# Performance work log

Hardware: AMD Instinct MI355X
Metric: run time of the kernel (lower is better)

Reference implementation:

```python
import jax, jax.numpy as jnp
import numpy as np

N_NODES = 50000
EMB = 256
HEADS = 8
NEG_SLOPE = 0.2


def gat_conv(x, src, dst, W, a_src, a_dst, b, num_nodes):
    # x: [N, Din]; W: [Din, H, F]; a_src/a_dst: [H, F]; b: [H*F]
    h = jnp.einsum('nd,dhf->nhf', x, W)                      # [N, H, F]
    al_s = jnp.sum(h * a_src, axis=-1)                       # [N, H]
    al_d = jnp.sum(h * a_dst, axis=-1)                       # [N, H]
    logits = jax.nn.leaky_relu(al_s[src] + al_d[dst], NEG_SLOPE)  # [E, H]
    # segment softmax over incoming edges of each destination node
    m = jax.ops.segment_max(logits, dst, num_segments=num_nodes)  # [N, H]
    e = jnp.exp(logits - m[dst])                              # [E, H]
    z = jax.ops.segment_sum(e, dst, num_segments=num_nodes)   # [N, H]
    alpha = e / (z[dst] + 1e-16)                              # [E, H]
    msg = h[src] * alpha[..., None]                           # [E, H, F]
    out = jax.ops.segment_sum(msg, dst, num_segments=num_nodes)  # [N, H, F]
    return out.reshape(num_nodes, -1) + b


def setup_inputs() -> dict:
    key = jax.random.key(0)
    ks = jax.random.split(key, 10)
    F1 = EMB // HEADS  # 32
    x = jax.random.normal(ks[0], (N_NODES, EMB), dtype=jnp.float32)
    edge_index = jax.random.randint(ks[1], (2, 800000), 0, N_NODES, dtype=jnp.int64)
    s1 = 1.0 / np.sqrt(EMB)
    W1 = jax.random.normal(ks[2], (EMB, HEADS, F1), dtype=jnp.float32) * s1
    a_src1 = jax.random.normal(ks[3], (HEADS, F1), dtype=jnp.float32) * s1
    a_dst1 = jax.random.normal(ks[4], (HEADS, F1), dtype=jnp.float32) * s1
    b1 = jnp.zeros((HEADS * F1,), dtype=jnp.float32)
    W2 = jax.random.normal(ks[5], (EMB, 1, EMB), dtype=jnp.float32) * s1
    a_src2 = jax.random.normal(ks[6], (1, EMB), dtype=jnp.float32) * s1
    a_dst2 = jax.random.normal(ks[7], (1, EMB), dtype=jnp.float32) * s1
    b2 = jnp.zeros((EMB,), dtype=jnp.float32)
    return {"x": x, "edge_index": edge_index,
            "W1": W1, "a_src1": a_src1, "a_dst1": a_dst1, "b1": b1,
            "W2": W2, "a_src2": a_src2, "a_dst2": a_dst2, "b2": b2}


def reference(x, edge_index, W1, a_src1, a_dst1, b1, W2, a_src2, a_dst2, b2):
    n = x.shape[0]
    loops = jnp.arange(n, dtype=edge_index.dtype)
    src = jnp.concatenate([edge_index[0], loops])
    dst = jnp.concatenate([edge_index[1], loops])
    h = gat_conv(x, src, dst, W1, a_src1, a_dst1, b1, n)   # [N, EMB]
    out = gat_conv(h, src, dst, W2, a_src2, a_dst2, b2, n)  # [N, EMB]
    return out
```

## Files before the change

kernel.cpp:

```cpp
#include <hip/hip_runtime.h>
#include <hip/hip_bf16.h>

typedef unsigned short u16;
typedef unsigned int   u32;

typedef __attribute__((ext_vector_type(8))) short s16x8;
typedef __attribute__((ext_vector_type(8))) unsigned short u16x8;
typedef __attribute__((ext_vector_type(4))) float f32x4;

#define CAP 64

__device__ __forceinline__ float b2f(u16 u) {
    union { u32 i; float f; } v; v.i = ((u32)u) << 16; return v.f;
}
__device__ __forceinline__ u16 f2b(float f) {
    union { float f; u32 i; } v; v.f = f;
    u32 u = v.i;
    u32 r = (u + 0x7fffu + ((u >> 16) & 1u)) >> 16;
    return (u16)r;
}

__device__ __forceinline__ int detect_f32(const u16* xw) {
    int t = threadIdx.x & 63;
    u16 w = xw[2 * t];
    int e = (w >> 7) & 0xFF;
    bool sane = (e >= 112 && e <= 131);
    unsigned long long m1 = __ballot(sane);
    return (__popcll(m1) >= 32) ? 0 : 1;
}

__device__ __forceinline__ int edge_at(const int* __restrict__ ei, int i64f, long long j) {
    return i64f ? ei[2 * j] : ei[(size_t)j];
}

__device__ __forceinline__ u16x8 loadA8(const void* __restrict__ A, size_t eoff, int f32f) {
    if (f32f) {
        const float* p = (const float*)A + eoff;
        float4 v0 = *(const float4*)p;
        float4 v1 = *(const float4*)(p + 4);
        u16x8 r;
        r[0] = f2b(v0.x); r[1] = f2b(v0.y); r[2] = f2b(v0.z); r[3] = f2b(v0.w);
        r[4] = f2b(v1.x); r[5] = f2b(v1.y); r[6] = f2b(v1.z); r[7] = f2b(v1.w);
        return r;
    }
    return *(const u16x8*)((const u16*)A + eoff);
}

__global__ __launch_bounds__(256) void prep(const void* __restrict__ x,
                                            const int* __restrict__ ei,
                                            const void* __restrict__ W1, const void* __restrict__ W2,
                                            const void* p0, const void* p1, const void* p2,
                                            const void* p3, const void* p4, const void* p5,
                                            u16* __restrict__ wt1, u16* __restrict__ wt2,
                                            u16* __restrict__ sv,
                                            int* __restrict__ cur, u16* __restrict__ csr,
                                            int* __restrict__ flags, u16* __restrict__ hp,
                                            int ZB, int CF, int NN) {
    int b = blockIdx.x, t = threadIdx.x;
    int f32f = detect_f32((const u16*)x);
    if (b < 512) {
        const void* W = (b < 256) ? W1 : W2;
        u16* Wt = (b < 256) ? wt1 : wt2;
        int k = b & 255;
        u16 v = f32f ? f2b(((const float*)W)[k * 256 + t]) : ((const u16*)W)[k * 256 + t];
        Wt[t * 256 + k] = v;
        return;
    }
    b -= 512;
    if (b == 0) {
        const void* ps[6] = {p0, p1, p2, p3, p4, p5};
#pragma unroll
        for (int j = 0; j < 6; j++) {
            u16 v = f32f ? f2b(((const float*)ps[j])[t]) : ((const u16*)ps[j])[t];
            sv[j * 256 + t] = v;
        }
        hp[(size_t)NN * 256 + t] = 0;
        if (t < 64) {
            bool hz = (ei[2 * t + 1] == 0);
            unsigned long long m2 = __ballot(hz);
            if (t == 0) {
                flags[0] = f32f;
                flags[1] = (m2 == ~0ull) ? 1 : 0;
            }
        }
        return;
    }
    b -= 1;
    if (b < ZB) {
        int i = b * 256 + t;
        if (i < (NN + 3) / 4) ((int4*)cur)[i] = make_int4(0, 0, 0, 0);
        return;
    }
    b -= ZB;
    if (b < CF) {
        int i = b * 256 + t;
        int pat = (NN & 0xFFFF) | (NN << 16);
        if (i < NN * (CAP / 8)) ((int4*)csr)[i] = make_int4(pat, pat, pat, pat);
        return;
    }
}

__global__ __launch_bounds__(256) void fill_csr(const int* __restrict__ ei,
                                                int* __restrict__ cur,
                                                u16* __restrict__ csr, int E, int ET,
                                                const int* __restrict__ flags) {
    int i = blockIdx.x * 256 + threadIdx.x;
    if (i >= ET) return;
    int i64f = flags[1];
    int s, d;
    if (i < E) { s = edge_at(ei, i64f, i); d = edge_at(ei, i64f, (long long)E + i); }
    else       { s = d = i - E; }
    int p = atomicAdd(&cur[d], 1);
    if (p < CAP) csr[d * CAP + p] = (u16)s;
}

__global__ __launch_bounds__(256) void gemm_tiled(const void* __restrict__ A,
                                                  const u16* __restrict__ Bt,
                                                  u16* __restrict__ C, int M,
                                                  const int* __restrict__ flags, int dynA) {
    __shared__ u16 sA[128 * 32];
    __shared__ u16 sB[128 * 32];
    int f32a = dynA ? flags[0] : 0;
    int tid = threadIdx.x;
    int mt = blockIdx.x >> 1, nt = blockIdx.x & 1;
    int r0 = mt * 128, c0 = nt * 128;
    int w = tid >> 6, lane = tid & 63;
    int wr = w & 1, wc = w >> 1;
    int lm = lane & 15, quad = lane >> 4;

    int row0 = tid >> 2, ch0 = tid & 3;
    int row1 = row0 + 64;
    int ga0 = r0 + row0; if (ga0 >= M) ga0 = M - 1;
    int ga1 = r0 + row1; if (ga1 >= M) ga1 = M - 1;
    size_t aoff0 = (size_t)ga0 * 256 + ch0 * 8;
    size_t aoff1 = (size_t)ga1 * 256 + ch0 * 8;
    const u16* Bb0 = Bt + (size_t)(c0 + row0) * 256 + ch0 * 8;
    const u16* Bb1 = Bt + (size_t)(c0 + row1) * 256 + ch0 * 8;

    u16x8 ra0 = loadA8(A, aoff0, f32a);
    u16x8 ra1 = loadA8(A, aoff1, f32a);
    u16x8 rb0 = *(const u16x8*)Bb0;
    u16x8 rb1 = *(const u16x8*)Bb1;

    f32x4 acc[4][4];
#pragma unroll
    for (int i = 0; i < 4; i++)
#pragma unroll
        for (int j = 0; j < 4; j++) acc[i][j] = (f32x4){0.f, 0.f, 0.f, 0.f};

    u16* wA0 = sA + row0 * 32 + ch0 * 8;
    u16* wA1 = sA + row1 * 32 + ch0 * 8;
    u16* wB0 = sB + row0 * 32 + ch0 * 8;
    u16* wB1 = sB + row1 * 32 + ch0 * 8;
    const u16* rA = sA + (wr * 64 + lm) * 32 + quad * 8;
    const u16* rB = sB + (wc * 64 + lm) * 32 + quad * 8;

    for (int kb = 0; kb < 8; kb++) {
        __syncthreads();
        *(u16x8*)wA0 = ra0;
        *(u16x8*)wA1 = ra1;
        *(u16x8*)wB0 = rb0;
        *(u16x8*)wB1 = rb1;
        __syncthreads();
        if (kb < 7) {
            int ko = (kb + 1) * 32;
            ra0 = loadA8(A, aoff0 + ko, f32a);
            ra1 = loadA8(A, aoff1 + ko, f32a);
            rb0 = *(const u16x8*)(Bb0 + ko);
            rb1 = *(const u16x8*)(Bb1 + ko);
        }
        s16x8 af[4], bf[4];
#pragma unroll
        for (int fr = 0; fr < 4; fr++) af[fr] = *(const s16x8*)(rA + fr * 16 * 32);
#pragma unroll
        for (int fc = 0; fc < 4; fc++) bf[fc] = *(const s16x8*)(rB + fc * 16 * 32);
#pragma unroll
        for (int fr = 0; fr < 4; fr++)
#pragma unroll
            for (int fc = 0; fc < 4; fc++)
                acc[fr][fc] = __builtin_amdgcn_mfma_f32_16x16x32_bf16(af[fr], bf[fc], acc[fr][fc], 0, 0, 0);
    }

#pragma unroll
    for (int fr = 0; fr < 4; fr++) {
#pragma unroll
        for (int fc = 0; fc < 4; fc++) {
#pragma unroll
            for (int r = 0; r < 4; r++) {
                int row = r0 + wr * 64 + fr * 16 + quad * 4 + r;
                if (row < M) C[(size_t)row * 256 + c0 + wc * 64 + fc * 16 + lm] = f2b(acc[fr][fc][r]);
            }
        }
    }
}

__global__ __launch_bounds__(256) void coeff256(const u16* __restrict__ h,
                                                const u16* __restrict__ a_s,
                                                const u16* __restrict__ a_d,
                                                float* __restrict__ al_s,
                                                float* __restrict__ al_d, int N, int H) {
    int tid = threadIdx.x;
    if (blockIdx.x == 0 && tid < 8) al_s[(size_t)N * H + tid] = -1e30f;
    int wid = tid >> 6, lane = tid & 63;
    int node = blockIdx.x * 4 + wid;
    if (node >= N) return;
    ushort4 hv = *(const ushort4*)(h + (size_t)node * 256 + lane * 4);
    ushort4 as = *(const ushort4*)(a_s + lane * 4);
    ushort4 ad = *(const ushort4*)(a_d + lane * 4);
    float h0 = b2f(hv.x), h1 = b2f(hv.y), h2 = b2f(hv.z), h3 = b2f(hv.w);
    float ps = h0 * b2f(as.x) + h1 * b2f(as.y) + h2 * b2f(as.z) + h3 * b2f(as.w);
    float pd = h0 * b2f(ad.x) + h1 * b2f(ad.y) + h2 * b2f(ad.z) + h3 * b2f(ad.w);
    int gsz = 64 / H;
    for (int m = 1; m < gsz; m <<= 1) {
        ps += __shfl_xor(ps, m, 64);
        pd += __shfl_xor(pd, m, 64);
    }
    if ((lane & (gsz - 1)) == 0) {
        int hh = lane / gsz;
        al_s[(size_t)node * H + hh] = ps;
        al_d[(size_t)node * H + hh] = pd;
    }
}

template <int H, int FINAL>
__global__ __launch_bounds__(256) void gat_agg(const u16* __restrict__ hsrc,
                                               const float* __restrict__ al_s,
                                               const float* __restrict__ al_d,
                                               const int* __restrict__ degv,
                                               const u16* __restrict__ csr16,
                                               const u16* __restrict__ bias,
                                               u16* __restrict__ out_b16,
                                               void* __restrict__ out_final,
                                               const int* __restrict__ flags, int N) {
    int wid = threadIdx.x >> 6, lane = threadIdx.x & 63;
    int c = lane * 4;
    int hc = (H == 8) ? (lane >> 3) : 0;
    int he = lane & (H - 1);
    int j8 = lane >> 3;
    const u16* hb = hsrc + c;
    ushort4 bv = *(const ushort4*)(bias + c);
    int f32f = FINAL ? flags[0] : 0;
    int step = gridDim.x * 8;

    for (int n0 = blockIdx.x * 8 + wid * 2; n0 < N; n0 += step) {
        int nA = n0, nB = n0 + 1;
        int hasB = (nB < N) ? 1 : 0;
        int degA = degv[nA]; degA = degA < CAP ? degA : CAP;
        int degB = hasB ? degv[nB] : 0; degB = degB < CAP ? degB : CAP;
        int padA = (degA + 7) & ~7;
        int padB = (degB + 7) & ~7;
        const u16* cA = csr16 + nA * CAP;
        const u16* cB = csr16 + nB * CAP;
        float adA = al_d[(size_t)nA * H + he];
        float adB = hasB ? al_d[(size_t)nB * H + he] : 0.f;

        float aA0 = 0.f, aA1 = 0.f, aA2 = 0.f, aA3 = 0.f, zA = 0.f;
        float aB0 = 0.f, aB1 = 0.f, aB2 = 0.f, aB3 = 0.f, zB = 0.f;

        int gmax = padA > padB ? padA : padB;
        for (int g = 0; g < gmax; g += 8) {
            int doA = g < padA, doB = g < padB;
            if (doA & doB) {
                int smA = cA[g + j8];
                int smB = cB[g + j8];
                float vA = al_s[(size_t)smA * H + he] + adA;
                float vB = al_s[(size_t)smB * H + he] + adB;
                vA = vA > 0.f ? vA : 0.2f * vA;
                vB = vB > 0.f ? vB : 0.2f * vB;
                float eA = __expf(vA);
                float eB = __expf(vB);
#pragma unroll
                for (int j = 0; j < 8; j++) {
                    int   sjA = __shfl(smA, j * 8, 64);
                    int   sjB = __shfl(smB, j * 8, 64);
                    float ejA = __shfl(eA, j * 8 + hc, 64);
                    float ejB = __shfl(eB, j * 8 + hc, 64);
                    ushort4 hvA = *(const ushort4*)(hb + (size_t)sjA * 256);
                    ushort4 hvB = *(const ushort4*)(hb + (size_t)sjB * 256);
                    zA += ejA;
                    aA0 += ejA * b2f(hvA.x); aA1 += ejA * b2f(hvA.y);
                    aA2 += ejA * b2f(hvA.z); aA3 += ejA * b2f(hvA.w);
                    zB += ejB;
                    aB0 += ejB * b2f(hvB.x); aB1 += ejB * b2f(hvB.y);
                    aB2 += ejB * b2f(hvB.z); aB3 += ejB * b2f(hvB.w);
                }
            } else if (doA) {
                int sm = cA[g + j8];
                float v = al_s[(size_t)sm * H + he] + adA;
                v = v > 0.f ? v : 0.2f * v;
                float e = __expf(v);
#pragma unroll
                for (int j = 0; j < 8; j++) {
                    int   sj = __shfl(sm, j * 8, 64);
                    float ej = __shfl(e, j * 8 + hc, 64);
                    ushort4 hv = *(const ushort4*)(hb + (size_t)sj * 256);
                    zA += ej;
                    aA0 += ej * b2f(hv.x); aA1 += ej * b2f(hv.y);
                    aA2 += ej * b2f(hv.z); aA3 += ej * b2f(hv.w);
                }
            } else {
                int sm = cB[g + j8];
                float v = al_s[(size_t)sm * H + he] + adB;
                v = v > 0.f ? v : 0.2f * v;
                float e = __expf(v);
#pragma unroll
                for (int j = 0; j < 8; j++) {
                    int   sj = __shfl(sm, j * 8, 64);
                    float ej = __shfl(e, j * 8 + hc, 64);
                    ushort4 hv = *(const ushort4*)(hb + (size_t)sj * 256);
                    zB += ej;
                    aB0 += ej * b2f(hv.x); aB1 += ej * b2f(hv.y);
                    aB2 += ej * b2f(hv.z); aB3 += ej * b2f(hv.w);
                }
            }
        }

        {
            float invz = 1.f / (zA + 1e-16f);
            float o0 = aA0 * invz + b2f(bv.x);
            float o1 = aA1 * invz + b2f(bv.y);
            float o2 = aA2 * invz + b2f(bv.z);
            float o3 = aA3 * invz + b2f(bv.w);
            if (FINAL) {
                if (f32f) {
                    float4 ov; ov.x = o0; ov.y = o1; ov.z = o2; ov.w = o3;
                    ((float4*)out_final)[(size_t)nA * 64 + lane] = ov;
                } else {
                    ushort4 ov; ov.x = f2b(o0); ov.y = f2b(o1); ov.z = f2b(o2); ov.w = f2b(o3);
                    ((ushort4*)out_final)[(size_t)nA * 64 + lane] = ov;
                }
            } else {
                ushort4 ov; ov.x = f2b(o0); ov.y = f2b(o1); ov.z = f2b(o2); ov.w = f2b(o3);
                ((ushort4*)out_b16)[(size_t)nA * 64 + lane] = ov;
            }
        }
        if (hasB) {
            float invz = 1.f / (zB + 1e-16f);
            float o0 = aB0 * invz + b2f(bv.x);
            float o1 = aB1 * invz + b2f(bv.y);
            float o2 = aB2 * invz + b2f(bv.z);
            float o3 = aB3 * invz + b2f(bv.w);
            if (FINAL) {
                if (f32f) {
                    float4 ov; ov.x = o0; ov.y = o1; ov.z = o2; ov.w = o3;
                    ((float4*)out_final)[(size_t)nB * 64 + lane] = ov;
                } else {
                    ushort4 ov; ov.x = f2b(o0); ov.y = f2b(o1); ov.z = f2b(o2); ov.w = f2b(o3);
                    ((ushort4*)out_final)[(size_t)nB * 64 + lane] = ov;
                }
            } else {
                ushort4 ov; ov.x = f2b(o0); ov.y = f2b(o1); ov.z = f2b(o2); ov.w = f2b(o3);
                ((ushort4*)out_b16)[(size_t)nB * 64 + lane] = ov;
            }
        }
    }
}

extern "C" void kernel_launch(void* const* d_in, const int* in_sizes, int n_in,
                              void* d_out, int out_size, void* d_ws, size_t ws_size,
                              hipStream_t stream) {
    (void)n_in; (void)out_size; (void)ws_size;
    const void* x   = d_in[0];
    const int*  ei  = (const int*)d_in[1];
    const void* W1  = d_in[2];
    const void* as1 = d_in[3];
    const void* ad1 = d_in[4];
    const void* b1  = d_in[5];
    const void* W2  = d_in[6];
    const void* as2 = d_in[7];
    const void* ad2 = d_in[8];
    const void* b2  = d_in[9];

    const int N  = in_sizes[0] / 256;
    const int E  = in_sizes[1] / 2;
    const int ET = E + N;

    char* base = (char*)d_ws;
    size_t o = 0;
    auto carve = [&](size_t bytes) -> void* {
        void* q = base + o;
        o += (bytes + 255) & ~(size_t)255;
        return q;
    };
    u16*   hproj = (u16*)carve((size_t)(N + 1) * 256 * 2);
    float* als   = (float*)carve((size_t)(N + 1) * 8 * 4);
    float* ald   = (float*)carve((size_t)N * 8 * 4);
    int*   cur   = (int*)carve(((size_t)N + 16) * 4);
    u16*   csr   = (u16*)carve((size_t)N * CAP * 2);
    u16*   wt1   = (u16*)carve(256 * 256 * 2);
    u16*   wt2   = (u16*)carve(256 * 256 * 2);
    u16*   sv    = (u16*)carve(6 * 256 * 2);
    int*   flags = (int*)carve(16 * 4);

    u16* xb = (u16*)d_out;

    int ZB = ((N + 3) / 4 + 255) / 256;
    int CF = (N * (CAP / 8) + 255) / 256;
    int PB = 512 + 1 + ZB + CF;
    prep<<<PB, 256, 0, stream>>>(x, ei, W1, W2, as1, ad1, b1, as2, ad2, b2,
                                 wt1, wt2, sv, cur, csr, flags, hproj,
                                 ZB, CF, N);

    int cg = (ET + 255) / 256;
    fill_csr<<<cg, 256, 0, stream>>>(ei, cur, csr, E, ET, flags);

    int gt = ((N + 127) / 128) * 2;
    int ab = (N + 3) / 4;
    int agb = 2048;
    gemm_tiled<<<gt, 256, 0, stream>>>(x, wt1, hproj, N, flags, 1);
    coeff256<<<ab, 256, 0, stream>>>(hproj, sv + 0 * 256, sv + 1 * 256, als, ald, N, 8);
    gat_agg<8, 0><<<agb, 256, 0, stream>>>(hproj, als, ald, cur, csr, sv + 2 * 256,
                                           xb, nullptr, flags, N);
    gemm_tiled<<<gt, 256, 0, stream>>>(xb, wt2, hproj, N, flags, 0);
    coeff256<<<ab, 256, 0, stream>>>(hproj, sv + 3 * 256, sv + 4 * 256, als, ald, N, 1);
    gat_agg<1, 1><<<agb, 256, 0, stream>>>(hproj, als, ald, cur, csr, sv + 5 * 256,
                                           nullptr, d_out, flags, N);
}
```

Before: 370.2 us.

## Fold attention coefficients into GEMM via precomputed W·a and merge CSR fill

Precomputes W·a_src and W·a_dst in prep, then computes the per-node attention logits as an extra MFMA column tile inside the projection GEMM, removing the separate coeff256 kernels and their reread of h. The CSR fill is folded into the first GEMM launch as extra blocks, removing a launch. The coefficients are now taken from bf16-rounded W·a products rather than from rounded h, which slightly changes numerics. The single prep block also does a serial 256-wide dot-product loop per thread.

Result: no change. 373.6 us (+0.9%).

```diff
diff --git a/kernel.cpp b/kernel.cpp
--- a/kernel.cpp
+++ b/kernel.cpp
@@ -55,6 +55,7 @@
                                             u16* __restrict__ sv,
                                             int* __restrict__ cur, u16* __restrict__ csr,
                                             int* __restrict__ flags, u16* __restrict__ hp,
+                                            u16* __restrict__ wsd1t, u16* __restrict__ wsd2t,
                                             int ZB, int CF, int NN) {
     int b = blockIdx.x, t = threadIdx.x;
     int f32f = detect_f32((const u16*)x);
@@ -75,6 +76,41 @@
             sv[j * 256 + t] = v;
         }
         hp[(size_t)NN * 256 + t] = 0;
+        {
+            int k = t;
+            for (int h = 0; h < 8; h++) {
+                float s = 0.f, d = 0.f;
+                for (int f0 = 0; f0 < 32; f0 += 8) {
+                    int idx = h * 32 + f0;
+                    u16x8 wv = loadA8(W1, (size_t)k * 256 + idx, f32f);
+                    u16x8 av = loadA8(p0, idx, f32f);
+                    u16x8 dv = loadA8(p1, idx, f32f);
+#pragma unroll
+                    for (int j = 0; j < 8; j++) {
+                        float w = b2f(wv[j]);
+                        s += w * b2f(av[j]);
+                        d += w * b2f(dv[j]);
+                    }
+                }
+                wsd1t[h * 256 + k] = f2b(s);
+                wsd1t[(8 + h) * 256 + k] = f2b(d);
+            }
+            float s2 = 0.f, d2 = 0.f;
+            for (int f0 = 0; f0 < 256; f0 += 8) {
+                u16x8 wv = loadA8(W2, (size_t)k * 256 + f0, f32f);
+                u16x8 av = loadA8(p3, f0, f32f);
+                u16x8 dv = loadA8(p4, f0, f32f);
+#pragma unroll
+                for (int j = 0; j < 8; j++) {
+                    float w = b2f(wv[j]);
+                    s2 += w * b2f(av[j]);
+                    d2 += w * b2f(dv[j]);
+                }
+            }
+            for (int cc = 0; cc < 16; cc++) wsd2t[cc * 256 + k] = 0;
+            wsd2t[k] = f2b(s2);
+            wsd2t[8 * 256 + k] = f2b(d2);
+        }
         if (t < 64) {
             bool hz = (ei[2 * t + 1] == 0);
             unsigned long long m2 = __ballot(hz);
@@ -100,26 +136,34 @@
     }
 }
 
-__global__ __launch_bounds__(256) void fill_csr(const int* __restrict__ ei,
-                                                int* __restrict__ cur,
-                                                u16* __restrict__ csr, int E, int ET,
-                                                const int* __restrict__ flags) {
-    int i = blockIdx.x * 256 + threadIdx.x;
-    if (i >= ET) return;
-    int i64f = flags[1];
-    int s, d;
-    if (i < E) { s = edge_at(ei, i64f, i); d = edge_at(ei, i64f, (long long)E + i); }
-    else       { s = d = i - E; }
-    int p = atomicAdd(&cur[d], 1);
-    if (p < CAP) csr[d * CAP + p] = (u16)s;
-}
-
 __global__ __launch_bounds__(256) void gemm_tiled(const void* __restrict__ A,
                                                   const u16* __restrict__ Bt,
                                                   u16* __restrict__ C, int M,
-                                                  const int* __restrict__ flags, int dynA) {
+                                                  const int* __restrict__ flags, int dynA,
+                                                  const u16* __restrict__ wsdT,
+                                                  float* __restrict__ als,
+                                                  float* __restrict__ ald, int H,
+                                                  const int* __restrict__ ei,
+                                                  int* __restrict__ cur,
+                                                  u16* __restrict__ csr,
+                                                  int E, int ET, int gtA) {
     __shared__ u16 sA[128 * 32];
     __shared__ u16 sB[128 * 32];
+    if ((int)blockIdx.x >= gtA) {
+        int i = (blockIdx.x - gtA) * 256 + threadIdx.x;
+        if (i < ET) {
+            int i64f = flags[1];
+            int s, d;
+            if (i < E) { s = edge_at(ei, i64f, i); d = edge_at(ei, i64f, (long long)E + i); }
+            else       { s = d = i - E; }
+            int p = atomicAdd(&cur[d], 1);
+            if (p < CAP) csr[d * CAP + p] = (u16)s;
+        }
+        return;
+    }
+    if (blockIdx.x == 0 && threadIdx.x < (unsigned)H)
+        als[(size_t)M * H + threadIdx.x] = -1e30f;
+
     int f32a = dynA ? flags[0] : 0;
     int tid = threadIdx.x;
     int mt = blockIdx.x >> 1, nt = blockIdx.x & 1;
@@ -127,6 +171,7 @@
     int w = tid >> 6, lane = tid & 63;
     int wr = w & 1, wc = w >> 1;
     int lm = lane & 15, quad = lane >> 4;
+    bool doE = (nt == 0) && (w < 2);
 
     int row0 = tid >> 2, ch0 = tid & 3;
     int row1 = row0 + 64;
@@ -147,6 +192,9 @@
     for (int i = 0; i < 4; i++)
 #pragma unroll
         for (int j = 0; j < 4; j++) acc[i][j] = (f32x4){0.f, 0.f, 0.f, 0.f};
+    f32x4 acc_e[4];
+#pragma unroll
+    for (int i = 0; i < 4; i++) acc_e[i] = (f32x4){0.f, 0.f, 0.f, 0.f};
 
     u16* wA0 = sA + row0 * 32 + ch0 * 8;
     u16* wA1 = sA + row1 * 32 + ch0 * 8;
@@ -179,6 +227,12 @@
 #pragma unroll
             for (int fc = 0; fc < 4; fc++)
                 acc[fr][fc] = __builtin_amdgcn_mfma_f32_16x16x32_bf16(af[fr], bf[fc], acc[fr][fc], 0, 0, 0);
+        if (doE) {
+            s16x8 bfe = *(const s16x8*)(wsdT + (size_t)lm * 256 + kb * 32 + quad * 8);
+#pragma unroll
+            for (int fr = 0; fr < 4; fr++)
+                acc_e[fr] = __builtin_amdgcn_mfma_f32_16x16x32_bf16(af[fr], bfe, acc_e[fr], 0, 0, 0);
+        }
     }
 
 #pragma unroll
@@ -192,33 +246,24 @@
             }
         }
     }
-}
-
-__global__ __launch_bounds__(256) void coeff256(const u16* __restrict__ h,
-                                                const u16* __restrict__ a_s,
-                                                const u16* __restrict__ a_d,
-                                                float* __restrict__ al_s,
-                                                float* __restrict__ al_d, int N, int H) {
-    int tid = threadIdx.x;
-    if (blockIdx.x == 0 && tid < 8) al_s[(size_t)N * H + tid] = -1e30f;
-    int wid = tid >> 6, lane = tid & 63;
-    int node = blockIdx.x * 4 + wid;
-    if (node >= N) return;
-    ushort4 hv = *(const ushort4*)(h + (size_t)node * 256 + lane * 4);
-    ushort4 as = *(const ushort4*)(a_s + lane * 4);
-    ushort4 ad = *(const ushort4*)(a_d + lane * 4);
-    float h0 = b2f(hv.x), h1 = b2f(hv.y), h2 = b2f(hv.z), h3 = b2f(hv.w);
-    float ps = h0 * b2f(as.x) + h1 * b2f(as.y) + h2 * b2f(as.z) + h3 * b2f(as.w);
-    float pd = h0 * b2f(ad.x) + h1 * b2f(ad.y) + h2 * b2f(ad.z) + h3 * b2f(ad.w);
-    int gsz = 64 / H;
-    for (int m = 1; m < gsz; m <<= 1) {
-        ps += __shfl_xor(ps, m, 64);
-        pd += __shfl_xor(pd, m, 64);
-    }
-    if ((lane & (gsz - 1)) == 0) {
-        int hh = lane / gsz;
-        al_s[(size_t)node * H + hh] = ps;
-        al_d[(size_t)node * H + hh] = pd;
+    if (doE) {
+#pragma unroll
+        for (int fr = 0; fr < 4; fr++) {
+#pragma unroll
+            for (int r = 0; r < 4; r++) {
+                int row = r0 + wr * 64 + fr * 16 + quad * 4 + r;
+                if (row < M) {
+                    float v = acc_e[fr][r];
+                    if (H == 8) {
+                        if (lm < 8) als[(size_t)row * 8 + lm] = v;
+                        else        ald[(size_t)row * 8 + (lm - 8)] = v;
+                    } else {
+                        if (lm == 0)      als[row] = v;
+                        else if (lm == 8) ald[row] = v;
+                    }
+                }
+            }
+        }
     }
 }
 
@@ -390,6 +435,8 @@
     u16*   wt1   = (u16*)carve(256 * 256 * 2);
     u16*   wt2   = (u16*)carve(256 * 256 * 2);
     u16*   sv    = (u16*)carve(6 * 256 * 2);
+    u16*   wsd1t = (u16*)carve(16 * 256 * 2);
+    u16*   wsd2t = (u16*)carve(16 * 256 * 2);
     int*   flags = (int*)carve(16 * 4);
 
     u16* xb = (u16*)d_out;
@@ -399,20 +446,19 @@
     int PB = 512 + 1 + ZB + CF;
     prep<<<PB, 256, 0, stream>>>(x, ei, W1, W2, as1, ad1, b1, as2, ad2, b2,
                                  wt1, wt2, sv, cur, csr, flags, hproj,
-                                 ZB, CF, N);
-
+                                 wsd1t, wsd2t, ZB, CF, N);
+
+    int gt = ((N + 127) / 128) * 2;
     int cg = (ET + 255) / 256;
-    fill_csr<<<cg, 256, 0, stream>>>(ei, cur, csr, E, ET, flags);
-
-    int gt = ((N + 127) / 128) * 2;
-    int ab = (N + 3) / 4;
     int agb = 2048;
-    gemm_tiled<<<gt, 256, 0, stream>>>(x, wt1, hproj, N, flags, 1);
-    coeff256<<<ab, 256, 0, stream>>>(hproj, sv + 0 * 256, sv + 1 * 256, als, ald, N, 8);
+    gemm_tiled<<<gt + cg, 256, 0, stream>>>(x, wt1, hproj, N, flags, 1,
+                                            wsd1t, als, ald, 8,
+                                            ei, cur, csr, E, ET, gt);
     gat_agg<8, 0><<<agb, 256, 0, stream>>>(hproj, als, ald, cur, csr, sv + 2 * 256,
                                            xb, nullptr, flags, N);
-    gemm_tiled<<<gt, 256, 0, stream>>>(xb, wt2, hproj, N, flags, 0);
-    coeff256<<<ab, 256, 0, stream>>>(hproj, sv + 3 * 256, sv + 4 * 256, als, ald, N, 1);
+    gemm_tiled<<<gt, 256, 0, stream>>>(xb, wt2, hproj, N, flags, 0,
+                                       wsd2t, als, ald, 1,
+                                       ei, cur, csr, 0, 0, gt);
     gat_agg<1, 1><<<agb, 256, 0, stream>>>(hproj, als, ald, cur, csr, sv + 5 * 256,
                                            nullptr, d_out, flags, N);
 }
```

## Pre-convert x to bf16 in prep and load GEMM tiles directly to LDS

Applied to the files above, without the earlier changes.

The prep kernel gains extra blocks that convert the input x to a bf16 copy (stored in the output buffer), so the first GEMM no longer converts fp32 on the fly. The GEMM kernel drops its register-staged prefetch and instead issues global_load_lds 16-byte transfers straight into shared memory. This removes the per-thread conversion and LDS store instructions, but it adds a full pass over x in prep and loses the overlap the register prefetch gave between the next tile's loads and the current MFMAs.

New measurement: 359.7 us. 2.9% less time.

```diff
diff --git a/kernel.cpp b/kernel.cpp
--- a/kernel.cpp
+++ b/kernel.cpp
@@ -18,6 +18,11 @@
     u32 u = v.i;
     u32 r = (u + 0x7fffu + ((u >> 16) & 1u)) >> 16;
     return (u16)r;
+}
+
+__device__ __forceinline__ void glds16(const u16* g, u16* l) {
+    __builtin_amdgcn_global_load_lds((const __attribute__((address_space(1))) void*)g,
+                                     (__attribute__((address_space(3))) void*)l, 16, 0, 0);
 }
 
 __device__ __forceinline__ int detect_f32(const u16* xw) {
@@ -33,31 +38,31 @@
     return i64f ? ei[2 * j] : ei[(size_t)j];
 }
 
-__device__ __forceinline__ u16x8 loadA8(const void* __restrict__ A, size_t eoff, int f32f) {
-    if (f32f) {
-        const float* p = (const float*)A + eoff;
-        float4 v0 = *(const float4*)p;
-        float4 v1 = *(const float4*)(p + 4);
-        u16x8 r;
-        r[0] = f2b(v0.x); r[1] = f2b(v0.y); r[2] = f2b(v0.z); r[3] = f2b(v0.w);
-        r[4] = f2b(v1.x); r[5] = f2b(v1.y); r[6] = f2b(v1.z); r[7] = f2b(v1.w);
-        return r;
-    }
-    return *(const u16x8*)((const u16*)A + eoff);
-}
-
 __global__ __launch_bounds__(256) void prep(const void* __restrict__ x,
                                             const int* __restrict__ ei,
                                             const void* __restrict__ W1, const void* __restrict__ W2,
                                             const void* p0, const void* p1, const void* p2,
                                             const void* p3, const void* p4, const void* p5,
-                                            u16* __restrict__ wt1, u16* __restrict__ wt2,
-                                            u16* __restrict__ sv,
+                                            u16* __restrict__ xb, u16* __restrict__ wt1,
+                                            u16* __restrict__ wt2, u16* __restrict__ sv,
                                             int* __restrict__ cur, u16* __restrict__ csr,
                                             int* __restrict__ flags, u16* __restrict__ hp,
-                                            int ZB, int CF, int NN) {
+                                            int x4, int BX, int ZB, int CF, int NN) {
     int b = blockIdx.x, t = threadIdx.x;
     int f32f = detect_f32((const u16*)x);
+    if (b < BX) {
+        int i = b * 256 + t;
+        if (i < x4) {
+            ushort4 o;
+            if (f32f) {
+                float4 v = ((const float4*)x)[i];
+                o.x = f2b(v.x); o.y = f2b(v.y); o.z = f2b(v.z); o.w = f2b(v.w);
+            } else o = ((const ushort4*)x)[i];
+            ((ushort4*)xb)[i] = o;
+        }
+        return;
+    }
+    b -= BX;
     if (b < 512) {
         const void* W = (b < 256) ? W1 : W2;
         u16* Wt = (b < 256) ? wt1 : wt2;
@@ -114,13 +119,11 @@
     if (p < CAP) csr[d * CAP + p] = (u16)s;
 }
 
-__global__ __launch_bounds__(256) void gemm_tiled(const void* __restrict__ A,
+__global__ __launch_bounds__(256) void gemm_tiled(const u16* __restrict__ A,
                                                   const u16* __restrict__ Bt,
-                                                  u16* __restrict__ C, int M,
-                                                  const int* __restrict__ flags, int dynA) {
+                                                  u16* __restrict__ C, int M) {
     __shared__ u16 sA[128 * 32];
     __shared__ u16 sB[128 * 32];
-    int f32a = dynA ? flags[0] : 0;
     int tid = threadIdx.x;
     int mt = blockIdx.x >> 1, nt = blockIdx.x & 1;
     int r0 = mt * 128, c0 = nt * 128;
@@ -128,47 +131,37 @@
     int wr = w & 1, wc = w >> 1;
     int lm = lane & 15, quad = lane >> 4;
 
-    int row0 = tid >> 2, ch0 = tid & 3;
-    int row1 = row0 + 64;
-    int ga0 = r0 + row0; if (ga0 >= M) ga0 = M - 1;
-    int ga1 = r0 + row1; if (ga1 >= M) ga1 = M - 1;
-    size_t aoff0 = (size_t)ga0 * 256 + ch0 * 8;
-    size_t aoff1 = (size_t)ga1 * 256 + ch0 * 8;
-    const u16* Bb0 = Bt + (size_t)(c0 + row0) * 256 + ch0 * 8;
-    const u16* Bb1 = Bt + (size_t)(c0 + row1) * 256 + ch0 * 8;
-
-    u16x8 ra0 = loadA8(A, aoff0, f32a);
-    u16x8 ra1 = loadA8(A, aoff1, f32a);
-    u16x8 rb0 = *(const u16x8*)Bb0;
-    u16x8 rb1 = *(const u16x8*)Bb1;
-
-    f32x4 acc[4][4];
-#pragma unroll
-    for (int i = 0; i < 4; i++)
-#pragma unroll
-        for (int j = 0; j < 4; j++) acc[i][j] = (f32x4){0.f, 0.f, 0.f, 0.f};
-
-    u16* wA0 = sA + row0 * 32 + ch0 * 8;
-    u16* wA1 = sA + row1 * 32 + ch0 * 8;
-    u16* wB0 = sB + row0 * 32 + ch0 * 8;
-    u16* wB1 = sB + row1 * 32 + ch0 * 8;
+    int sr0 = w * 16 + (lane >> 2);
+    int sr1 = 64 + w * 16 + (lane >> 2);
+    int sc  = (lane & 3) * 8;
+    int ga0 = r0 + sr0; if (ga0 >= M) ga0 = M - 1;
+    int ga1 = r0 + sr1; if (ga1 >= M) ga1 = M - 1;
+    const u16* Ag0 = A + (size_t)ga0 * 256 + sc;
+    const u16* Ag1 = A + (size_t)ga1 * 256 + sc;
+    const u16* Bg0 = Bt + (size_t)(c0 + sr0) * 256 + sc;
+    const u16* Bg1 = Bt + (size_t)(c0 + sr1) * 256 + sc;
+    u16* sA0 = sA + (w * 16) * 32;
+    u16* sA1 = sA + (64 + w * 16) * 32;
+    u16* sB0 = sB + (w * 16) * 32;
+    u16* sB1 = sB + (64 + w * 16) * 32;
+
     const u16* rA = sA + (wr * 64 + lm) * 32 + quad * 8;
     const u16* rB = sB + (wc * 64 + lm) * 32 + quad * 8;
 
+    f32x4 acc[4][4];
+#pragma unroll
+    for (int i = 0; i < 4; i++)
+#pragma unroll
+        for (int j = 0; j < 4; j++) acc[i][j] = (f32x4){0.f, 0.f, 0.f, 0.f};
+
     for (int kb = 0; kb < 8; kb++) {
+        int ko = kb * 32;
         __syncthreads();
-        *(u16x8*)wA0 = ra0;
-        *(u16x8*)wA1 = ra1;
-        *(u16x8*)wB0 = rb0;
-        *(u16x8*)wB1 = rb1;
+        glds16(Ag0 + ko, sA0);
+        glds16(Ag1 + ko, sA1);
+        glds16(Bg0 + ko, sB0);
+        glds16(Bg1 + ko, sB1);
         __syncthreads();
-        if (kb < 7) {
-            int ko = (kb + 1) * 32;
-            ra0 = loadA8(A, aoff0 + ko, f32a);
-            ra1 = loadA8(A, aoff1 + ko, f32a);
-            rb0 = *(const u16x8*)(Bb0 + ko);
-            rb1 = *(const u16x8*)(Bb1 + ko);
-        }
         s16x8 af[4], bf[4];
 #pragma unroll
         for (int fr = 0; fr < 4; fr++) af[fr] = *(const s16x8*)(rA + fr * 16 * 32);
@@ -394,12 +387,14 @@
 
     u16* xb = (u16*)d_out;
 
+    int x4 = N * 256 / 4;
+    int BX = (x4 + 255) / 256;
     int ZB = ((N + 3) / 4 + 255) / 256;
     int CF = (N * (CAP / 8) + 255) / 256;
-    int PB = 512 + 1 + ZB + CF;
+    int PB = BX + 512 + 1 + ZB + CF;
     prep<<<PB, 256, 0, stream>>>(x, ei, W1, W2, as1, ad1, b1, as2, ad2, b2,
-                                 wt1, wt2, sv, cur, csr, flags, hproj,
-                                 ZB, CF, N);
+                                 xb, wt1, wt2, sv, cur, csr, flags, hproj,
+                                 x4, BX, ZB, CF, N);
 
     int cg = (ET + 255) / 256;
     fill_csr<<<cg, 256, 0, stream>>>(ei, cur, csr, E, ET, flags);
@@ -407,11 +402,11 @@
     int gt = ((N + 127) / 128) * 2;
     int ab = (N + 3) / 4;
     int agb = 2048;
-    gemm_tiled<<<gt, 256, 0, stream>>>(x, wt1, hproj, N, flags, 1);
+    gemm_tiled<<<gt, 256, 0, stream>>>(xb, wt1, hproj, N);
     coeff256<<<ab, 256, 0, stream>>>(hproj, sv + 0 * 256, sv + 1 * 256, als, ald, N, 8);
     gat_agg<8, 0><<<agb, 256, 0, stream>>>(hproj, als, ald, cur, csr, sv + 2 * 256,
                                            xb, nullptr, flags, N);
-    gemm_tiled<<<gt, 256, 0, stream>>>(xb, wt2, hproj, N, flags, 0);
+    gemm_tiled<<<gt, 256, 0, stream>>>(xb, wt2, hproj, N);
     coeff256<<<ab, 256, 0, stream>>>(hproj, sv + 3 * 256, sv + 4 * 256, als, ald, N, 1);
     gat_agg<1, 1><<<agb, 256, 0, stream>>>(hproj, als, ald, cur, csr, sv + 5 * 256,
                                            nullptr, d_out, flags, N);
```
